# Kernel optimization log

Hardware: AMD Instinct MI355X
Metric: run time of the kernel (lower is better)

The kernel has to match this reference:

```python
import jax, jax.numpy as jnp
import numpy as np

B, K, D, DICT, C = 2048, 32, 768, 24576, 64


def setup_inputs() -> dict:
    key = jax.random.key(0)
    ks = jax.random.split(key, 9)
    up_vals = jax.random.uniform(ks[0], (B, K), dtype=jnp.float32)
    up_decoder_w = jax.random.normal(ks[1], (D, DICT), dtype=jnp.float32) * 0.02
    down_encoder_w = jax.random.normal(ks[2], (DICT, D), dtype=jnp.float32) * 0.02
    up_encoder_w = jax.random.normal(ks[3], (DICT, D), dtype=jnp.float32) * 0.02
    b_dec = jax.random.normal(ks[4], (D,), dtype=jnp.float32) * 0.02
    up_indices = jax.random.randint(ks[5], (B, K), 0, DICT)
    down_indices = jax.random.randint(ks[6], (B, K), 0, DICT)
    conn = jax.random.randint(ks[7], (DICT, C), 0, DICT)
    drop = jax.random.uniform(ks[8], (DICT, C)) < 0.1
    connections = jnp.where(drop, -1, conn)
    return {
        "up_vals": up_vals,
        "up_decoder_w": up_decoder_w,
        "down_encoder_w": down_encoder_w,
        "up_encoder_w": up_encoder_w,
        "b_dec": b_dec,
        "up_indices": up_indices,
        "down_indices": down_indices,
        "connections": connections,
    }


def reference(up_vals, up_decoder_w, down_encoder_w, up_encoder_w, b_dec,
              up_indices, down_indices, connections):
    # allowed upstream features per active downstream feature: [B, k_down, C]
    allowed = connections[down_indices]
    valid = allowed != -1
    # match[b,i,c,j] = allowed[b,i,c] == up_indices[b,j] (and slot valid)
    match = (allowed[..., None] == up_indices[:, None, None, :]) & valid[..., None]
    # multiplicity of each (down i, up j) pair across the C slots: [B, k_down, k_up]
    mult = match.sum(axis=2).astype(up_vals.dtype)
    # gather active decoder/encoder vectors
    act_up = up_decoder_w.T[up_indices]          # [B, k_up, D]
    act_down = down_encoder_w[down_indices]      # [B, k_down, D]
    # virtual weights between active down and up features
    vw = jnp.einsum('bid,bjd->bij', act_down, act_up)  # [B, k_down, k_up]
    contributions = jnp.einsum('bij,bij->bi', vw, mult * up_vals[:, None, :])
    # bias contribution (note: indexed by up_indices, broadcast add as in source)
    b_dec_contrib = up_encoder_w @ b_dec         # [DICT]
    return contributions + b_dec_contrib[up_indices]
```

## Files before the change

kernel.cpp:

```cpp
#include <hip/hip_runtime.h>

#define B_    2048
#define K_    32
#define D_    768
#define DICT_ 24576
#define C_    64

__global__ void transpose_kernel(const float* __restrict__ A, float* __restrict__ T) {
    __shared__ float tile[32][33];
    int x = blockIdx.x * 32 + threadIdx.x;
    #pragma unroll
    for (int k = 0; k < 4; ++k) {
        int y = blockIdx.y * 32 + threadIdx.y + k * 8;
        tile[threadIdx.y + k * 8][threadIdx.x] = A[(size_t)y * DICT_ + x];
    }
    __syncthreads();
    int tx = blockIdx.y * 32 + threadIdx.x;
    #pragma unroll
    for (int k = 0; k < 4; ++k) {
        int ty = blockIdx.x * 32 + threadIdx.y + k * 8;
        T[(size_t)ty * D_ + tx] = tile[threadIdx.x][threadIdx.y + k * 8];
    }
}

__global__ void bdc_kernel(const float* __restrict__ up_enc,
                           const float* __restrict__ b_dec,
                           float* __restrict__ bdc) {
    int wave = threadIdx.x >> 6;
    int lane = threadIdx.x & 63;
    int row  = blockIdx.x * 4 + wave;
    const float4* rp = (const float4*)(up_enc + (size_t)row * D_);
    const float4* bp = (const float4*)b_dec;
    float acc = 0.f;
    #pragma unroll
    for (int i = 0; i < 3; ++i) {
        float4 a = rp[lane + 64 * i];
        float4 b = bp[lane + 64 * i];
        acc += a.x * b.x + a.y * b.y + a.z * b.z + a.w * b.w;
    }
    #pragma unroll
    for (int off = 32; off; off >>= 1) acc += __shfl_xor(acc, off);
    if (lane == 0) bdc[row] = acc;
}

__global__ void main_kernel(const float* __restrict__ up_vals,
                            const float* __restrict__ up_dec,
                            const float* __restrict__ down_enc,
                            const float* __restrict__ up_enc,
                            const float* __restrict__ b_dec,
                            const int*   __restrict__ up_idx,
                            const int*   __restrict__ down_idx,
                            const int*   __restrict__ conn,
                            const float* __restrict__ T,
                            const float* __restrict__ bdc,
                            float* __restrict__ out) {
    int wave = threadIdx.x >> 6;
    int lane = threadIdx.x & 63;
    int item = blockIdx.x * 4 + wave;
    int b    = item >> 5;

    int di = down_idx[item];
    int allowed = conn[(size_t)di * C_ + lane];
    bool valid = allowed >= 0;
    int   myup  = up_idx[b * K_ + (lane & 31)];
    float myval = up_vals[b * K_ + (lane & 31)];

    const float* drow = down_enc + (size_t)di * D_;
    float acc = 0.f;

    #pragma unroll 1
    for (int j = 0; j < K_; ++j) {
        int tgt = __shfl(myup, j);
        unsigned long long m = __ballot(valid && (allowed == tgt));
        if (m != 0) {
            float w = (float)__popcll(m) * __shfl(myval, j);
            float partial = 0.f;
            if (T) {
                const float4* cp = (const float4*)(T + (size_t)tgt * D_);
                const float4* dp = (const float4*)drow;
                #pragma unroll
                for (int ii = 0; ii < 3; ++ii) {
                    float4 c = cp[lane + 64 * ii];
                    float4 d = dp[lane + 64 * ii];
                    partial += c.x * d.x + c.y * d.y + c.z * d.z + c.w * d.w;
                }
            } else {
                for (int d = lane; d < D_; d += 64)
                    partial += drow[d] * up_dec[(size_t)d * DICT_ + tgt];
            }
            acc += w * partial;
        }
    }

    if (!bdc) {
        int ui = up_idx[item];
        const float4* rp = (const float4*)(up_enc + (size_t)ui * D_);
        const float4* bp = (const float4*)b_dec;
        #pragma unroll
        for (int ii = 0; ii < 3; ++ii) {
            float4 a  = rp[lane + 64 * ii];
            float4 bb = bp[lane + 64 * ii];
            acc += a.x * bb.x + a.y * bb.y + a.z * bb.z + a.w * bb.w;
        }
    }

    #pragma unroll
    for (int off = 32; off; off >>= 1) acc += __shfl_xor(acc, off);
    if (lane == 0) {
        float bias = bdc ? bdc[up_idx[item]] : 0.f;
        out[item] = acc + bias;
    }
}

extern "C" void kernel_launch(void* const* d_in, const int* in_sizes, int n_in,
                              void* d_out, int out_size, void* d_ws, size_t ws_size,
                              hipStream_t stream) {
    (void)in_sizes; (void)n_in; (void)out_size;
    const float* up_vals  = (const float*)d_in[0];
    const float* up_dec   = (const float*)d_in[1];
    const float* down_enc = (const float*)d_in[2];
    const float* up_enc   = (const float*)d_in[3];
    const float* b_dec    = (const float*)d_in[4];
    const int*   up_idx   = (const int*)d_in[5];
    const int*   down_idx = (const int*)d_in[6];
    const int*   conn     = (const int*)d_in[7];
    float* out = (float*)d_out;

    size_t bdc_bytes = (size_t)DICT_ * sizeof(float);
    size_t T_bytes   = (size_t)DICT_ * D_ * sizeof(float);
    float* bdc = (ws_size >= bdc_bytes) ? (float*)d_ws : nullptr;
    float* T   = (ws_size >= bdc_bytes + T_bytes) ? (float*)d_ws + DICT_ : nullptr;

    if (T) {
        dim3 grid(DICT_ / 32, D_ / 32);
        transpose_kernel<<<grid, dim3(32, 8), 0, stream>>>(up_dec, T);
    }
    if (bdc) {
        bdc_kernel<<<DICT_ / 4, 256, 0, stream>>>(up_enc, b_dec, bdc);
    }
    main_kernel<<<(B_ * K_) / 4, 256, 0, stream>>>(up_vals, up_dec, down_enc, up_enc,
                                                   b_dec, up_idx, down_idx, conn,
                                                   T, bdc, out);
}
```

Before: 265.1 us.

## Drop full decoder transpose and bias precompute; fuse into single gather kernel

Removes the kernel that transposed the entire up_decoder matrix into workspace and the kernel that precomputed the bias dot product for every dictionary row. The main kernel now reads decoder columns directly with strided loads, only for the rare matched pairs, and computes the bias dot product inline per item. This avoids moving the full decoder matrix through memory twice, in exchange for uncoalesced column gathers and redundant per-item bias row reads.

```diff
diff --git a/kernel.cpp b/kernel.cpp
--- a/kernel.cpp
+++ b/kernel.cpp
@@ -6,67 +6,38 @@
 #define DICT_ 24576
 #define C_    64
 
-__global__ void transpose_kernel(const float* __restrict__ A, float* __restrict__ T) {
-    __shared__ float tile[32][33];
-    int x = blockIdx.x * 32 + threadIdx.x;
-    #pragma unroll
-    for (int k = 0; k < 4; ++k) {
-        int y = blockIdx.y * 32 + threadIdx.y + k * 8;
-        tile[threadIdx.y + k * 8][threadIdx.x] = A[(size_t)y * DICT_ + x];
-    }
-    __syncthreads();
-    int tx = blockIdx.y * 32 + threadIdx.x;
-    #pragma unroll
-    for (int k = 0; k < 4; ++k) {
-        int ty = blockIdx.x * 32 + threadIdx.y + k * 8;
-        T[(size_t)ty * D_ + tx] = tile[threadIdx.x][threadIdx.y + k * 8];
-    }
-}
+__global__ __launch_bounds__(256) void scae_fused_kernel(
+        const float* __restrict__ up_vals,
+        const float* __restrict__ up_dec,
+        const float* __restrict__ down_enc,
+        const float* __restrict__ up_enc,
+        const float* __restrict__ b_dec,
+        const int*   __restrict__ up_idx,
+        const int*   __restrict__ down_idx,
+        const int*   __restrict__ conn,
+        float* __restrict__ out) {
+    const int wave = threadIdx.x >> 6;
+    const int lane = threadIdx.x & 63;
+    const int item = blockIdx.x * 4 + wave;
+    const int b    = item >> 5;
 
-__global__ void bdc_kernel(const float* __restrict__ up_enc,
-                           const float* __restrict__ b_dec,
-                           float* __restrict__ bdc) {
-    int wave = threadIdx.x >> 6;
-    int lane = threadIdx.x & 63;
-    int row  = blockIdx.x * 4 + wave;
-    const float4* rp = (const float4*)(up_enc + (size_t)row * D_);
+    const int ui = up_idx[item];
+    const float4* rp = (const float4*)(up_enc + (size_t)ui * D_);
     const float4* bp = (const float4*)b_dec;
     float acc = 0.f;
     #pragma unroll
-    for (int i = 0; i < 3; ++i) {
-        float4 a = rp[lane + 64 * i];
-        float4 b = bp[lane + 64 * i];
-        acc += a.x * b.x + a.y * b.y + a.z * b.z + a.w * b.w;
+    for (int ii = 0; ii < 3; ++ii) {
+        float4 a  = rp[lane + 64 * ii];
+        float4 bb = bp[lane + 64 * ii];
+        acc += a.x * bb.x + a.y * bb.y + a.z * bb.z + a.w * bb.w;
     }
-    #pragma unroll
-    for (int off = 32; off; off >>= 1) acc += __shfl_xor(acc, off);
-    if (lane == 0) bdc[row] = acc;
-}
 
-__global__ void main_kernel(const float* __restrict__ up_vals,
-                            const float* __restrict__ up_dec,
-                            const float* __restrict__ down_enc,
-                            const float* __restrict__ up_enc,
-                            const float* __restrict__ b_dec,
-                            const int*   __restrict__ up_idx,
-                            const int*   __restrict__ down_idx,
-                            const int*   __restrict__ conn,
-                            const float* __restrict__ T,
-                            const float* __restrict__ bdc,
-                            float* __restrict__ out) {
-    int wave = threadIdx.x >> 6;
-    int lane = threadIdx.x & 63;
-    int item = blockIdx.x * 4 + wave;
-    int b    = item >> 5;
-
-    int di = down_idx[item];
-    int allowed = conn[(size_t)di * C_ + lane];
-    bool valid = allowed >= 0;
-    int   myup  = up_idx[b * K_ + (lane & 31)];
-    float myval = up_vals[b * K_ + (lane & 31)];
-
+    const int di = down_idx[item];
+    const int allowed = conn[(size_t)di * C_ + lane];
+    const bool valid  = allowed >= 0;
+    const int   myup  = up_idx[b * K_ + (lane & 31)];
+    const float myval = up_vals[b * K_ + (lane & 31)];
     const float* drow = down_enc + (size_t)di * D_;
-    float acc = 0.f;
 
     #pragma unroll 1
     for (int j = 0; j < K_; ++j) {
@@ -75,47 +46,24 @@
         if (m != 0) {
             float w = (float)__popcll(m) * __shfl(myval, j);
             float partial = 0.f;
-            if (T) {
-                const float4* cp = (const float4*)(T + (size_t)tgt * D_);
-                const float4* dp = (const float4*)drow;
-                #pragma unroll
-                for (int ii = 0; ii < 3; ++ii) {
-                    float4 c = cp[lane + 64 * ii];
-                    float4 d = dp[lane + 64 * ii];
-                    partial += c.x * d.x + c.y * d.y + c.z * d.z + c.w * d.w;
-                }
-            } else {
-                for (int d = lane; d < D_; d += 64)
-                    partial += drow[d] * up_dec[(size_t)d * DICT_ + tgt];
+            #pragma unroll
+            for (int ii = 0; ii < 12; ++ii) {
+                int d = lane + 64 * ii;
+                partial += drow[d] * up_dec[(size_t)d * DICT_ + tgt];
             }
             acc += w * partial;
         }
     }
 
-    if (!bdc) {
-        int ui = up_idx[item];
-        const float4* rp = (const float4*)(up_enc + (size_t)ui * D_);
-        const float4* bp = (const float4*)b_dec;
-        #pragma unroll
-        for (int ii = 0; ii < 3; ++ii) {
-            float4 a  = rp[lane + 64 * ii];
-            float4 bb = bp[lane + 64 * ii];
-            acc += a.x * bb.x + a.y * bb.y + a.z * bb.z + a.w * bb.w;
-        }
-    }
-
     #pragma unroll
     for (int off = 32; off; off >>= 1) acc += __shfl_xor(acc, off);
-    if (lane == 0) {
-        float bias = bdc ? bdc[up_idx[item]] : 0.f;
-        out[item] = acc + bias;
-    }
+    if (lane == 0) out[item] = acc;
 }
 
 extern "C" void kernel_launch(void* const* d_in, const int* in_sizes, int n_in,
                               void* d_out, int out_size, void* d_ws, size_t ws_size,
                               hipStream_t stream) {
-    (void)in_sizes; (void)n_in; (void)out_size;
+    (void)in_sizes; (void)n_in; (void)out_size; (void)d_ws; (void)ws_size;
     const float* up_vals  = (const float*)d_in[0];
     const float* up_dec   = (const float*)d_in[1];
     const float* down_enc = (const float*)d_in[2];
@@ -126,19 +74,6 @@
     const int*   conn     = (const int*)d_in[7];
     float* out = (float*)d_out;
 
-    size_t bdc_bytes = (size_t)DICT_ * sizeof(float);
-    size_t T_bytes   = (size_t)DICT_ * D_ * sizeof(float);
-    float* bdc = (ws_size >= bdc_bytes) ? (float*)d_ws : nullptr;
-    float* T   = (ws_size >= bdc_bytes + T_bytes) ? (float*)d_ws + DICT_ : nullptr;
-
-    if (T) {
-        dim3 grid(DICT_ / 32, D_ / 32);
-        transpose_kernel<<<grid, dim3(32, 8), 0, stream>>>(up_dec, T);
-    }
-    if (bdc) {
-        bdc_kernel<<<DICT_ / 4, 256, 0, stream>>>(up_enc, b_dec, bdc);
-    }
-    main_kernel<<<(B_ * K_) / 4, 256, 0, stream>>>(up_vals, up_dec, down_enc, up_enc,
-                                                   b_dec, up_idx, down_idx, conn,
-                                                   T, bdc, out);
+    scae_fused_kernel<<<(B_ * K_) / 4, 256, 0, stream>>>(
+        up_vals, up_dec, down_enc, up_enc, b_dec, up_idx, down_idx, conn, out);
 }
```

Result: no change. 270.3 us (+2.0%).

## Replace full decoder transpose with sparse match list and strided pair dots

Applied to the files above, without the earlier changes.

Removes the transpose of the whole 24576x768 up-decoder matrix, which costs a 75MB read and write on every call. A match kernel now records each (item, up feature, weight) pair into a compacted list using an atomic counter and writes the bias to the output. A grid-stride pairdot kernel then computes each dot product straight from the column-strided decoder and atomically adds it to the output. This trades a large dense copy for uncoalesced strided reads on the few matched pairs, plus atomic contention and an extra launch.

```diff
diff --git a/kernel.cpp b/kernel.cpp
--- a/kernel.cpp
+++ b/kernel.cpp
@@ -6,26 +6,13 @@
 #define DICT_ 24576
 #define C_    64
 
-__global__ void transpose_kernel(const float* __restrict__ A, float* __restrict__ T) {
-    __shared__ float tile[32][33];
-    int x = blockIdx.x * 32 + threadIdx.x;
-    #pragma unroll
-    for (int k = 0; k < 4; ++k) {
-        int y = blockIdx.y * 32 + threadIdx.y + k * 8;
-        tile[threadIdx.y + k * 8][threadIdx.x] = A[(size_t)y * DICT_ + x];
-    }
-    __syncthreads();
-    int tx = blockIdx.y * 32 + threadIdx.x;
-    #pragma unroll
-    for (int k = 0; k < 4; ++k) {
-        int ty = blockIdx.x * 32 + threadIdx.y + k * 8;
-        T[(size_t)ty * D_ + tx] = tile[threadIdx.x][threadIdx.y + k * 8];
-    }
-}
+#define ENTRY_CAP (1 << 20)
 
-__global__ void bdc_kernel(const float* __restrict__ up_enc,
-                           const float* __restrict__ b_dec,
-                           float* __restrict__ bdc) {
+__global__ __launch_bounds__(256) void bdc_kernel(const float* __restrict__ up_enc,
+                                                  const float* __restrict__ b_dec,
+                                                  float* __restrict__ bdc,
+                                                  int* __restrict__ count) {
+    if (blockIdx.x == 0 && threadIdx.x == 0) *count = 0;
     int wave = threadIdx.x >> 6;
     int lane = threadIdx.x & 63;
     int row  = blockIdx.x * 4 + wave;
@@ -43,31 +30,97 @@
     if (lane == 0) bdc[row] = acc;
 }
 
-__global__ void main_kernel(const float* __restrict__ up_vals,
-                            const float* __restrict__ up_dec,
-                            const float* __restrict__ down_enc,
-                            const float* __restrict__ up_enc,
-                            const float* __restrict__ b_dec,
-                            const int*   __restrict__ up_idx,
-                            const int*   __restrict__ down_idx,
-                            const int*   __restrict__ conn,
-                            const float* __restrict__ T,
-                            const float* __restrict__ bdc,
-                            float* __restrict__ out) {
+__global__ __launch_bounds__(256) void match_kernel(const float* __restrict__ up_vals,
+                                                    const int*   __restrict__ up_idx,
+                                                    const int*   __restrict__ down_idx,
+                                                    const int*   __restrict__ conn,
+                                                    const float* __restrict__ bdc,
+                                                    int*  __restrict__ count,
+                                                    int4* __restrict__ entries,
+                                                    float* __restrict__ out) {
+    int wave = threadIdx.x >> 6;
+    int lane = threadIdx.x & 63;
+    int item = blockIdx.x * 4 + wave;
+    int b    = __builtin_amdgcn_readfirstlane(item >> 5);
+
+    int di = down_idx[item];
+    int allowed = conn[(size_t)di * C_ + lane];
+    bool valid  = allowed >= 0;
+
+    const int*   ub = up_idx  + (size_t)b * K_;
+    const float* vb = up_vals + (size_t)b * K_;
+
+    #pragma unroll 1
+    for (int j = 0; j < K_; ++j) {
+        int tgt = __builtin_amdgcn_readfirstlane(ub[j]);
+        unsigned long long m = __ballot(valid && (allowed == tgt));
+        if (m != 0) {
+            if (lane == 0) {
+                float w = (float)__popcll(m) * vb[j];
+                int idx = atomicAdd(count, 1);
+                if (idx < ENTRY_CAP)
+                    entries[idx] = make_int4(item, tgt, __float_as_int(w), 0);
+            }
+        }
+    }
+    if (lane == 0) out[item] = bdc[up_idx[item]];
+}
+
+__global__ __launch_bounds__(256) void pairdot_kernel(const float* __restrict__ up_dec,
+                                                      const float* __restrict__ down_enc,
+                                                      const int*   __restrict__ down_idx,
+                                                      const int*   __restrict__ count,
+                                                      const int4*  __restrict__ entries,
+                                                      float* __restrict__ out) {
+    int lane   = threadIdx.x & 63;
+    int gwave  = (blockIdx.x * blockDim.x + threadIdx.x) >> 6;
+    int nwaves = (gridDim.x * blockDim.x) >> 6;
+    int n = *count;
+    if (n > ENTRY_CAP) n = ENTRY_CAP;
+
+    for (int e = gwave; e < n; e += nwaves) {
+        int4 ent = entries[e];
+        int item = ent.x, tgt = ent.y;
+        float w  = __int_as_float(ent.z);
+        int di   = down_idx[item];
+        const float* drow = down_enc + (size_t)di * D_;
+        float p = 0.f;
+        #pragma unroll
+        for (int ii = 0; ii < 12; ++ii) {
+            int d = lane + 64 * ii;
+            p += drow[d] * up_dec[(size_t)d * DICT_ + tgt];
+        }
+        #pragma unroll
+        for (int off = 32; off; off >>= 1) p += __shfl_xor(p, off);
+        if (lane == 0) atomicAdd(&out[item], w * p);
+    }
+}
+
+__global__ __launch_bounds__(256) void scae_fused_kernel(
+        const float* __restrict__ up_vals, const float* __restrict__ up_dec,
+        const float* __restrict__ down_enc, const float* __restrict__ up_enc,
+        const float* __restrict__ b_dec, const int* __restrict__ up_idx,
+        const int* __restrict__ down_idx, const int* __restrict__ conn,
+        float* __restrict__ out) {
     int wave = threadIdx.x >> 6;
     int lane = threadIdx.x & 63;
     int item = blockIdx.x * 4 + wave;
     int b    = item >> 5;
-
+    int ui = up_idx[item];
+    const float4* rp = (const float4*)(up_enc + (size_t)ui * D_);
+    const float4* bp = (const float4*)b_dec;
+    float acc = 0.f;
+    #pragma unroll
+    for (int ii = 0; ii < 3; ++ii) {
+        float4 a = rp[lane + 64 * ii]; float4 bb = bp[lane + 64 * ii];
+        acc += a.x * bb.x + a.y * bb.y + a.z * bb.z + a.w * bb.w;
+    }
     int di = down_idx[item];
     int allowed = conn[(size_t)di * C_ + lane];
     bool valid = allowed >= 0;
-    int   myup  = up_idx[b * K_ + (lane & 31)];
+    int myup = up_idx[b * K_ + (lane & 31)];
     float myval = up_vals[b * K_ + (lane & 31)];
-
     const float* drow = down_enc + (size_t)di * D_;
-    float acc = 0.f;
-
     #pragma unroll 1
     for (int j = 0; j < K_; ++j) {
         int tgt = __shfl(myup, j);
@@ -75,41 +128,17 @@
         if (m != 0) {
             float w = (float)__popcll(m) * __shfl(myval, j);
             float partial = 0.f;
-            if (T) {
-                const float4* cp = (const float4*)(T + (size_t)tgt * D_);
-                const float4* dp = (const float4*)drow;
-                #pragma unroll
-                for (int ii = 0; ii < 3; ++ii) {
-                    float4 c = cp[lane + 64 * ii];
-                    float4 d = dp[lane + 64 * ii];
-                    partial += c.x * d.x + c.y * d.y + c.z * d.z + c.w * d.w;
-                }
-            } else {
-                for (int d = lane; d < D_; d += 64)
-                    partial += drow[d] * up_dec[(size_t)d * DICT_ + tgt];
+            #pragma unroll
+            for (int ii = 0; ii < 12; ++ii) {
+                int d = lane + 64 * ii;
+                partial += drow[d] * up_dec[(size_t)d * DICT_ + tgt];
             }
             acc += w * partial;
         }
     }
-
-    if (!bdc) {
-        int ui = up_idx[item];
-        const float4* rp = (const float4*)(up_enc + (size_t)ui * D_);
-        const float4* bp = (const float4*)b_dec;
-        #pragma unroll
-        for (int ii = 0; ii < 3; ++ii) {
-            float4 a  = rp[lane + 64 * ii];
-            float4 bb = bp[lane + 64 * ii];
-            acc += a.x * bb.x + a.y * bb.y + a.z * bb.z + a.w * bb.w;
-        }
-    }
-
     #pragma unroll
     for (int off = 32; off; off >>= 1) acc += __shfl_xor(acc, off);
-    if (lane == 0) {
-        float bias = bdc ? bdc[up_idx[item]] : 0.f;
-        out[item] = acc + bias;
-    }
+    if (lane == 0) out[item] = acc;
 }
 
 extern "C" void kernel_launch(void* const* d_in, const int* in_sizes, int n_in,
@@ -126,19 +155,20 @@
     const int*   conn     = (const int*)d_in[7];
     float* out = (float*)d_out;
 
-    size_t bdc_bytes = (size_t)DICT_ * sizeof(float);
-    size_t T_bytes   = (size_t)DICT_ * D_ * sizeof(float);
-    float* bdc = (ws_size >= bdc_bytes) ? (float*)d_ws : nullptr;
-    float* T   = (ws_size >= bdc_bytes + T_bytes) ? (float*)d_ws + DICT_ : nullptr;
+    size_t need = 256 + (size_t)DICT_ * 4 + (size_t)ENTRY_CAP * 16;
+    if (ws_size < need) {
+        scae_fused_kernel<<<(B_ * K_) / 4, 256, 0, stream>>>(
+            up_vals, up_dec, down_enc, up_enc, b_dec, up_idx, down_idx, conn, out);
+        return;
+    }
 
-    if (T) {
-        dim3 grid(DICT_ / 32, D_ / 32);
-        transpose_kernel<<<grid, dim3(32, 8), 0, stream>>>(up_dec, T);
-    }
-    if (bdc) {
-        bdc_kernel<<<DICT_ / 4, 256, 0, stream>>>(up_enc, b_dec, bdc);
-    }
-    main_kernel<<<(B_ * K_) / 4, 256, 0, stream>>>(up_vals, up_dec, down_enc, up_enc,
-                                                   b_dec, up_idx, down_idx, conn,
-                                                   T, bdc, out);
+    int*   count   = (int*)d_ws;
+    float* bdc     = (float*)((char*)d_ws + 256);
+    int4*  entries = (int4*)((char*)d_ws + 256 + (size_t)DICT_ * 4);
+
+    bdc_kernel<<<DICT_ / 4, 256, 0, stream>>>(up_enc, b_dec, bdc, count);
+    match_kernel<<<(B_ * K_) / 4, 256, 0, stream>>>(up_vals, up_idx, down_idx, conn,
+                                                    bdc, count, entries, out);
+    pairdot_kernel<<<1024, 256, 0, stream>>>(up_dec, down_enc, down_idx,
+                                             count, entries, out);
 }
```

New measurement: 323.5 us. 22.0% more time.
